# Kernel optimization log

Hardware: AMD Instinct MI355X
Metric: run time of the kernel (lower is better)

## Reference

```python
import jax, jax.numpy as jnp
import numpy as np

B, S, H = 8, 4096, 1024
E, K = 64, 2
CAP_FACTOR = 1.25
TEMP = 1.0
LBW = 0.01


def setup_inputs() -> dict:
    key = jax.random.key(0)
    k1, k2, k3 = jax.random.split(key, 3)
    x = jax.random.normal(k1, (B, S, H), dtype=jnp.float32)
    gate_w = jax.random.normal(k2, (E, H), dtype=jnp.float32) * 0.02
    expert_w = jax.random.normal(k3, (E, H, H), dtype=jnp.float32) * 0.02
    return {"x": x, "gate_w": gate_w, "expert_w": expert_w}


def _moe_forward(x, gate_w, expert_w):
    b, s, h = x.shape
    xf = x.reshape(-1, h)                      # [N, H]
    N = xf.shape[0]
    capacity = int(N * K / E * CAP_FACTOR)

    # --- gating ---
    logits = xf @ gate_w.T                     # [N, E]
    vals, idx = jax.lax.top_k(logits / TEMP, K)  # [N, K]
    probs = jax.nn.softmax(vals, axis=-1)      # [N, K]

    # --- dispatch: first-come-first-served position within each expert ---
    ef = idx.reshape(-1)                       # [N*K], token-major order (matches torch loop)
    onehot = jax.nn.one_hot(ef, E, dtype=jnp.int32)            # [N*K, E]
    pos = jnp.take_along_axis(jnp.cumsum(onehot, axis=0), ef[:, None], axis=1)[:, 0] - 1
    valid = pos < capacity
    slot = jnp.where(valid, ef * capacity + pos, E * capacity)  # out-of-range -> dropped

    # token_map[e, c] = token_idx * K + k  (or -1 if empty)
    token_map = jnp.full((E * capacity,), -1, dtype=jnp.int32)
    token_map = token_map.at[slot].set(jnp.arange(N * K, dtype=jnp.int32), mode="drop")

    tok = jnp.clip(token_map // K, 0, N - 1)
    filled = token_map >= 0
    expert_inputs = jnp.where(filled[:, None], xf[tok], 0.0)    # [E*cap, H]
    expert_inputs = expert_inputs.reshape(E, capacity, h)

    # --- grouped expert GEMM (no bias; zero rows stay zero) ---
    expert_outputs = jnp.einsum("ech,edh->ecd", expert_inputs, expert_w)  # [E, cap, H]

    # --- combine: weighted scatter-add back to tokens ---
    eo_flat = expert_outputs.reshape(E * capacity, h)
    wk = token_map % K
    weight = jnp.where(filled, probs[tok, jnp.clip(wk, 0, K - 1)], 0.0)
    out_idx = jnp.where(filled, tok, N)        # invalid -> dropped
    output = jnp.zeros((N, h), dtype=xf.dtype).at[out_idx].add(
        weight[:, None] * eo_flat, mode="drop")

    # --- aux load-balancing loss ---
    gate_probs = jax.nn.softmax(logits, axis=-1)
    usage = jnp.bincount(ef, length=E).astype(jnp.float32) / (N * K + 1e-9)
    importance = gate_probs.mean(axis=0)
    aux = jnp.sum(usage * importance) * E
    aux = jnp.minimum(aux * LBW, 1.0)

    return output.reshape(b, s, h), aux


def reference(x, gate_w, expert_w):
    return _moe_forward(x, gate_w, expert_w)
```

## Files before the change

### kernel.cpp

```cpp
#include <hip/hip_runtime.h>
#include <hip/hip_bf16.h>

#define NTOK 32768
#define NE 64
#define HD 1024
#define CAP 1280
#define NKF (NTOK*2)
#define NSLOT (NE*CAP)
#define NTILE 128

typedef __attribute__((ext_vector_type(8))) short bf16x8;
typedef __attribute__((ext_vector_type(4))) short bf16x4;
typedef __attribute__((ext_vector_type(4))) float f32x4;
typedef __attribute__((ext_vector_type(4))) unsigned short u16x4;

__device__ __hip_bfloat16 g_zero[1152];

__device__ __forceinline__ short f2bf(float f) {
  union { __hip_bfloat16 b; short s; } u;
  u.b = __float2bfloat16(f);
  return u.s;
}
__device__ __forceinline__ float bf2f(unsigned short h) {
  return __uint_as_float(((unsigned)h) << 16);
}

__global__ __launch_bounds__(256) void gating_kernel(const float* __restrict__ x,
                                                     const float* __restrict__ gw,
                                                     float* __restrict__ logits,
                                                     __hip_bfloat16* __restrict__ xb) {
  __shared__ float Xs[64][132];
  __shared__ float Gs[64][132];
  const int tid = threadIdx.x;
  const int tok0 = blockIdx.x * 64;
  const int th = tid >> 4;
  const int te = tid & 15;
  float acc[4][4];
#pragma unroll
  for (int i = 0; i < 4; ++i)
#pragma unroll
    for (int j = 0; j < 4; ++j) acc[i][j] = 0.f;

  for (int k0 = 0; k0 < HD; k0 += 128) {
#pragma unroll
    for (int r = 0; r < 8; ++r) {
      int idx = r * 256 + tid;
      int row = idx >> 5;
      int c = (idx & 31) * 4;
      float4 xv4 = *(const float4*)&x[(size_t)(tok0 + row) * HD + k0 + c];
      *(float4*)&Xs[row][c] = xv4;
      bf16x4 o;
      o[0] = f2bf(xv4.x); o[1] = f2bf(xv4.y); o[2] = f2bf(xv4.z); o[3] = f2bf(xv4.w);
      *(bf16x4*)&xb[(size_t)(tok0 + row) * HD + k0 + c] = o;
      *(float4*)&Gs[row][c] = *(const float4*)&gw[(size_t)row * HD + k0 + c];
    }
    __syncthreads();
#pragma unroll 4
    for (int kk = 0; kk < 32; ++kk) {
      float4 xv[4], gv[4];
#pragma unroll
      for (int i = 0; i < 4; ++i) xv[i] = *(float4*)&Xs[th + i * 16][kk * 4];
#pragma unroll
      for (int j = 0; j < 4; ++j) gv[j] = *(float4*)&Gs[te + j * 16][kk * 4];
#pragma unroll
      for (int i = 0; i < 4; ++i)
#pragma unroll
        for (int j = 0; j < 4; ++j) {
          acc[i][j] = fmaf(xv[i].x, gv[j].x, acc[i][j]);
          acc[i][j] = fmaf(xv[i].y, gv[j].y, acc[i][j]);
          acc[i][j] = fmaf(xv[i].z, gv[j].z, acc[i][j]);
          acc[i][j] = fmaf(xv[i].w, gv[j].w, acc[i][j]);
        }
    }
    __syncthreads();
  }
#pragma unroll
  for (int i = 0; i < 4; ++i)
#pragma unroll
    for (int j = 0; j < 4; ++j)
      logits[(size_t)(tok0 + th + i * 16) * NE + te + j * 16] = acc[i][j];
}

__global__ __launch_bounds__(256) void topk_hist_kernel(const float* __restrict__ logits,
                                                        int2* __restrict__ e01,
                                                        float2* __restrict__ p01,
                                                        float* __restrict__ imp_part,
                                                        int* __restrict__ rank_buf,
                                                        int* __restrict__ hist) {
  __shared__ int wh[4][64];
  const int tid = threadIdx.x;
  const int w = tid >> 6, lane = tid & 63;
  const int t = blockIdx.x * 256 + tid;
  float l[64];
  const float4* lp = (const float4*)(logits + (size_t)t * NE);
#pragma unroll
  for (int i = 0; i < 16; ++i) {
    float4 v = lp[i];
    l[4 * i] = v.x; l[4 * i + 1] = v.y; l[4 * i + 2] = v.z; l[4 * i + 3] = v.w;
  }
  float v1 = -1e30f; int i1 = 0;
#pragma unroll
  for (int j = 0; j < 64; ++j) if (l[j] > v1) { v1 = l[j]; i1 = j; }
  float v2 = -1e30f; int i2 = 0;
#pragma unroll
  for (int j = 0; j < 64; ++j) if (j != i1 && l[j] > v2) { v2 = l[j]; i2 = j; }
  float ex = __expf(v2 - v1);
  float inv2 = 1.f / (1.f + ex);
  e01[t] = make_int2(i1, i2);
  p01[t] = make_float2(inv2, ex * inv2);

  float s = 0.f;
#pragma unroll
  for (int j = 0; j < 64; ++j) s += __expf(l[j] - v1);
  float invs = 1.f / s;
  const int wid = t >> 6;
#pragma unroll
  for (int e = 0; e < 64; ++e) {
    float p = __expf(l[e] - v1) * invs;
#pragma unroll
    for (int off = 32; off; off >>= 1) p += __shfl_xor(p, off);
    if (lane == 0) imp_part[(size_t)wid * 64 + e] = p;
  }

  int r0 = 0, r1 = 0, cnt = 0;
#pragma unroll
  for (int j = 0; j < 64; ++j) {
    int a = __shfl(i1, j);
    int b = __shfl(i2, j);
    int ja = (j < lane);
    r0 += ja & (a == i1);
    r0 += ja & (b == i1);
    r1 += ja & (a == i2);
    r1 += ja & (b == i2);
    cnt += (a == lane) + (b == lane);
  }
  wh[w][lane] = cnt;
  __syncthreads();
#pragma unroll
  for (int ww = 0; ww < 4; ++ww)
    if (ww < w) { r0 += wh[ww][i1]; r1 += wh[ww][i2]; }
  rank_buf[2 * t] = r0;
  rank_buf[2 * t + 1] = r1;
  if (tid < 64)
    hist[blockIdx.x * 64 + tid] = wh[0][tid] + wh[1][tid] + wh[2][tid] + wh[3][tid];
}

__global__ __launch_bounds__(64) void scan_aux_kernel(const int* __restrict__ hist,
                                                      const float* __restrict__ imp_part,
                                                      int* __restrict__ tile_off,
                                                      int* __restrict__ counts,
                                                      float* __restrict__ out) {
  const int e = threadIdx.x;
  int run = 0;
  for (int t = 0; t < NTILE; ++t) {
    int h = hist[t * 64 + e];
    tile_off[t * 64 + e] = run;
    run += h;
  }
  counts[e] = run;

  float imp = 0.f;
  for (int w = 0; w < 512; ++w) imp += imp_part[(size_t)w * 64 + e];
  imp *= (1.f / (float)NTOK);
  float usage = (float)run / (float)NKF;
  float v = usage * imp;
#pragma unroll
  for (int off = 32; off; off >>= 1) v += __shfl_xor(v, off);
  if (e == 0) out[(size_t)NTOK * HD] = fminf(v * (float)NE * 0.01f, 1.0f);
}

__global__ __launch_bounds__(256) void place_kernel(const int2* __restrict__ e01,
                                                    const int* __restrict__ rank_buf,
                                                    const int* __restrict__ tile_off,
                                                    int* __restrict__ slot_of,
                                                    int* __restrict__ slot_token) {
  const int tid = threadIdx.x;
  const int i = blockIdx.x * 256 + tid;
  int2 ee = e01[i >> 1];
  const int e = (i & 1) ? ee.y : ee.x;
  const int pos = tile_off[(i >> 9) * 64 + e] + rank_buf[i];
  const int slot = (pos < CAP) ? (e * CAP + pos) : -1;
  slot_of[i] = slot;
  if (slot >= 0) slot_token[slot] = i;
}

__global__ __launch_bounds__(256) void convw_kernel(const float* __restrict__ w,
                                                    __hip_bfloat16* __restrict__ wb) {
  size_t i = ((size_t)blockIdx.x * 256 + threadIdx.x) * 8;
  const size_t stride = (size_t)2048 * 256 * 8;
#pragma unroll 2
  for (int it = 0; it < 16; ++it, i += stride) {
    float4 a = *(const float4*)(w + i);
    float4 b = *(const float4*)(w + i + 4);
    bf16x8 o;
    o[0] = f2bf(a.x); o[1] = f2bf(a.y); o[2] = f2bf(a.z); o[3] = f2bf(a.w);
    o[4] = f2bf(b.x); o[5] = f2bf(b.y); o[6] = f2bf(b.z); o[7] = f2bf(b.w);
    *(bf16x8*)(wb + i) = o;
  }
}

#define ASYNC16(g, l) __builtin_amdgcn_global_load_lds( \
    (const __attribute__((address_space(1))) void*)(g), \
    (__attribute__((address_space(3))) void*)(l), 16, 0, 0)

#define STAGE_A(buf, ks, kcol) do {                                             \
    const int _d = ((buf) * 16384 + (ks) * 8192 + wuni) * 2;                    \
    ASYNC16(arow0 + (kcol) + (ks) * 32 + sw8, (char*)lds + _d);                 \
    ASYNC16(arow1 + (kcol) + (ks) * 32 + sw8, (char*)lds + _d + 8192);          \
  } while (0)

#define STAGE_B(buf, ks, kcol) do {                                             \
    const __hip_bfloat16* _g = B + (size_t)srow * HD + (kcol) + (ks) * 32 + sw8; \
    const int _d = (32768 + (buf) * 16384 + (ks) * 8192 + wuni) * 2;            \
    ASYNC16(_g, (char*)lds + _d);                                               \
    ASYNC16(_g + (size_t)128 * HD, (char*)lds + _d + 8192);                     \
  } while (0)

#define LDA(dst, buf, ks, mi) \
  dst = *(const bf16x8*)(lds + (buf) * 16384 + (ks) * 8192 + (wm * 128 + (mi) * 16 + fr) * 32 + rsw)
#define LDB(dst, buf, ks, ni) \
  dst = *(const bf16x8*)(lds + 32768 + (buf) * 16384 + (ks) * 8192 + (wn * 64 + (ni) * 16 + fr) * 32 + rsw)

#define MFMA_HALF(h)                                                            \
  _Pragma("unroll")                                                             \
  for (int mm = 0; mm < 4; ++mm)                                                \
    _Pragma("unroll")                                                           \
    for (int nn = 0; nn < 4; ++nn)                                              \
      acc[(h) * 4 + mm][nn] =                                                   \
          __builtin_amdgcn_mfma_f32_16x16x32_bf16(av[mm], bv[nn], acc[(h) * 4 + mm][nn], 0, 0, 0)

#define BARX() do { asm volatile("" ::: "memory"); __builtin_amdgcn_s_barrier(); asm volatile("" ::: "memory"); } while (0)

__global__ __launch_bounds__(512, 2) void moe_gemm_kernel(const __hip_bfloat16* __restrict__ xb,
                                                          const int* __restrict__ slot_token,
                                                          const __hip_bfloat16* __restrict__ Wb,
                                                          const int* __restrict__ counts,
                                                          __hip_bfloat16* __restrict__ Eo) {
  __shared__ __hip_bfloat16 lds[65536];

  const int bid = blockIdx.x;
  const int swz = (bid & 7) * 160 + (bid >> 3);
  const int e = swz / 20;
  const int t20 = swz - e * 20;
  const int tm = t20 >> 2, tn = t20 & 3;

  const int cnt = counts[e];
  if (tm * 256 >= cnt) return;

  const int tid = threadIdx.x;
  const int lane = tid & 63;
  const int w = tid >> 6;
  const int wm = w >> 2, wn = w & 3;

  const __hip_bfloat16* B = Wb + (size_t)e * HD * HD + (size_t)(tn * 256) * HD;

  const int srow = tid >> 2;
  const int sw8 = ((tid & 3) ^ ((tid >> 3) & 3)) * 8;
  const int wuni = w * 512;

  const int slotbase = e * CAP + tm * 256;
  const int r0row = tm * 256 + srow;
  const int i0 = slot_token[slotbase + srow];
  const int i1 = slot_token[slotbase + 128 + srow];
  const __hip_bfloat16* arow0 = (r0row < cnt) ? xb + (size_t)(i0 >> 1) * HD : g_zero;
  const __hip_bfloat16* arow1 = (r0row + 128 < cnt) ? xb + (size_t)(i1 >> 1) * HD : g_zero;

  const int fr = lane & 15;
  const int fq = lane >> 4;
  const int rsw = (fq ^ ((fr >> 1) & 3)) * 8;

  f32x4 acc[8][4] = {};

  STAGE_A(0, 0, 0);
  STAGE_B(0, 0, 0);
  STAGE_A(0, 1, 0);
  STAGE_B(0, 1, 0);
  asm volatile("s_waitcnt vmcnt(4)" ::: "memory");
  BARX();

#pragma unroll 2
  for (int t = 0; t < 16; ++t) {
    const int cur = t & 1, nxt = cur ^ 1;
    const int kc = (t + 1) * 64;
    const bool hn = (t < 15);
    bf16x8 av[4], bv[4];

    LDB(bv[0], cur, 0, 0); LDB(bv[1], cur, 0, 1); LDB(bv[2], cur, 0, 2); LDB(bv[3], cur, 0, 3);
    LDA(av[0], cur, 0, 0); LDA(av[1], cur, 0, 1); LDA(av[2], cur, 0, 2); LDA(av[3], cur, 0, 3);
    if (hn) STAGE_A(nxt, 0, kc);
    BARX();
    __builtin_amdgcn_s_setprio(1);
    MFMA_HALF(0);
    __builtin_amdgcn_s_setprio(0);
    BARX();

    LDA(av[0], cur, 0, 4); LDA(av[1], cur, 0, 5); LDA(av[2], cur, 0, 6); LDA(av[3], cur, 0, 7);
    if (hn) {
      STAGE_B(nxt, 0, kc);
      asm volatile("s_waitcnt vmcnt(4)" ::: "memory");
    } else {
      asm volatile("s_waitcnt vmcnt(0)" ::: "memory");
    }
    BARX();
    __builtin_amdgcn_s_setprio(1);
    MFMA_HALF(1);
    __builtin_amdgcn_s_setprio(0);
    BARX();

    LDB(bv[0], cur, 1, 0); LDB(bv[1], cur, 1, 1); LDB(bv[2], cur, 1, 2); LDB(bv[3], cur, 1, 3);
    LDA(av[0], cur, 1, 0); LDA(av[1], cur, 1, 1); LDA(av[2], cur, 1, 2); LDA(av[3], cur, 1, 3);
    if (hn) STAGE_A(nxt, 1, kc);
    BARX();
    __builtin_amdgcn_s_setprio(1);
    MFMA_HALF(0);
    __builtin_amdgcn_s_setprio(0);
    BARX();

    LDA(av[0], cur, 1, 4); LDA(av[1], cur, 1, 5); LDA(av[2], cur, 1, 6); LDA(av[3], cur, 1, 7);
    if (hn) {
      STAGE_B(nxt, 1, kc);
      asm volatile("s_waitcnt vmcnt(4)" ::: "memory");
    }
    BARX();
    __builtin_amdgcn_s_setprio(1);
    MFMA_HALF(1);
    __builtin_amdgcn_s_setprio(0);
    BARX();
  }

  __hip_bfloat16* C = Eo + (size_t)e * CAP * HD +
                      (size_t)(tm * 256 + wm * 128) * HD + tn * 256 + wn * 64;
#pragma unroll
  for (int m = 0; m < 8; ++m)
#pragma unroll
    for (int n = 0; n < 4; ++n)
#pragma unroll
      for (int r = 0; r < 4; ++r)
        C[(size_t)(m * 16 + fq * 4 + r) * HD + n * 16 + fr] = __float2bfloat16(acc[m][n][r]);
}

__global__ __launch_bounds__(256) void combine_kernel(const __hip_bfloat16* __restrict__ eo,
                                                      const int* __restrict__ slot_of,
                                                      const float2* __restrict__ p01,
                                                      float* __restrict__ out) {
  const int t = blockIdx.x;
  const int tid = threadIdx.x;
  const float2 p = p01[t];
  const int s0 = slot_of[2 * t], s1 = slot_of[2 * t + 1];
  float a0 = 0.f, a1 = 0.f, a2 = 0.f, a3 = 0.f;
  if (s0 >= 0) {
    u16x4 v = *(const u16x4*)((const unsigned short*)eo + (size_t)s0 * HD + tid * 4);
    a0 += p.x * bf2f(v[0]); a1 += p.x * bf2f(v[1]);
    a2 += p.x * bf2f(v[2]); a3 += p.x * bf2f(v[3]);
  }
  if (s1 >= 0) {
    u16x4 v = *(const u16x4*)((const unsigned short*)eo + (size_t)s1 * HD + tid * 4);
    a0 += p.y * bf2f(v[0]); a1 += p.y * bf2f(v[1]);
    a2 += p.y * bf2f(v[2]); a3 += p.y * bf2f(v[3]);
  }
  float4 res = make_float4(a0, a1, a2, a3);
  *(float4*)(out + (size_t)t * HD + tid * 4) = res;
}

extern "C" void kernel_launch(void* const* d_in, const int* in_sizes, int n_in,
                              void* d_out, int out_size, void* d_ws, size_t ws_size,
                              hipStream_t stream) {
  const float* x = (const float*)d_in[0];
  const float* gw = (const float*)d_in[1];
  const float* ew = (const float*)d_in[2];
  float* out = (float*)d_out;

  char* p = (char*)d_ws;
  float* logits = (float*)p;            p += (size_t)NTOK * NE * 4;
  int2* e01 = (int2*)p;                 p += (size_t)NTOK * 8;
  float2* p01 = (float2*)p;             p += (size_t)NTOK * 8;
  int* slot_of = (int*)p;               p += (size_t)NKF * 4;
  int* slot_token = (int*)p;            p += (size_t)NSLOT * 4;
  int* counts = (int*)p;                p += 256;
  float* imp_part = (float*)p;          p += (size_t)512 * 64 * 4;
  int* rank_buf = (int*)p;              p += (size_t)NKF * 4;
  int* hist = (int*)p;                  p += (size_t)NTILE * 64 * 4;
  int* tile_off = (int*)p;              p += (size_t)NTILE * 64 * 4;
  __hip_bfloat16* xb = (__hip_bfloat16*)p; p += (size_t)NTOK * HD * 2;
  __hip_bfloat16* Wb = (__hip_bfloat16*)p;  p += (size_t)NE * HD * HD * 2;
  __hip_bfloat16* Eo = (__hip_bfloat16*)p;  p += (size_t)NSLOT * HD * 2;

  gating_kernel<<<NTOK / 64, 256, 0, stream>>>(x, gw, logits, xb);
  topk_hist_kernel<<<NTOK / 256, 256, 0, stream>>>(logits, e01, p01, imp_part, rank_buf, hist);
  scan_aux_kernel<<<1, 64, 0, stream>>>(hist, imp_part, tile_off, counts, out);
  place_kernel<<<NKF / 256, 256, 0, stream>>>(e01, rank_buf, tile_off, slot_of, slot_token);
  convw_kernel<<<2048, 256, 0, stream>>>(ew, Wb);
  moe_gemm_kernel<<<dim3(1280), 512, 0, stream>>>(xb, slot_token, Wb, counts, Eo);
  combine_kernel<<<NTOK, 256, 0, stream>>>(Eo, slot_of, p01, out);
}
```

Baseline: 436.7 us.

## Triple-buffer expert weight tiles in LDS to prefetch two K-steps ahead

The B (expert weight) operand in the grouped expert GEMM moves from a double buffer to a three-slot ring in LDS. Weight loads are now issued two K-iterations ahead, while the gathered token rows (A) stay double-buffered one step ahead. The vmcnt wait counts are retuned for the deeper pipeline, including special handling of the last two iterations. This is meant to hide more of the global-load latency for the weights. In exchange, shared memory per block grows from 128 KB to 160 KB, which uses the whole CU's LDS, and the wait accounting becomes more fragile.

```diff
diff --git a/kernel.cpp b/kernel.cpp
--- a/kernel.cpp
+++ b/kernel.cpp
@@ -209,17 +209,17 @@
     ASYNC16(arow1 + (kcol) + (ks) * 32 + sw8, (char*)lds + _d + 8192);          \
   } while (0)
 
-#define STAGE_B(buf, ks, kcol) do {                                             \
+#define STAGE_B3(buf3, ks, kcol) do {                                           \
     const __hip_bfloat16* _g = B + (size_t)srow * HD + (kcol) + (ks) * 32 + sw8; \
-    const int _d = (32768 + (buf) * 16384 + (ks) * 8192 + wuni) * 2;            \
+    const int _d = (32768 + (buf3) * 16384 + (ks) * 8192 + wuni) * 2;           \
     ASYNC16(_g, (char*)lds + _d);                                               \
     ASYNC16(_g + (size_t)128 * HD, (char*)lds + _d + 8192);                     \
   } while (0)
 
 #define LDA(dst, buf, ks, mi) \
   dst = *(const bf16x8*)(lds + (buf) * 16384 + (ks) * 8192 + (wm * 128 + (mi) * 16 + fr) * 32 + rsw)
-#define LDB(dst, buf, ks, ni) \
-  dst = *(const bf16x8*)(lds + 32768 + (buf) * 16384 + (ks) * 8192 + (wn * 64 + (ni) * 16 + fr) * 32 + rsw)
+#define LDB3(dst, buf3, ks, ni) \
+  dst = *(const bf16x8*)(lds + 32768 + (buf3) * 16384 + (ks) * 8192 + (wn * 64 + (ni) * 16 + fr) * 32 + rsw)
 
 #define MFMA_HALF(h)                                                            \
   _Pragma("unroll")                                                             \
@@ -230,13 +230,14 @@
           __builtin_amdgcn_mfma_f32_16x16x32_bf16(av[mm], bv[nn], acc[(h) * 4 + mm][nn], 0, 0, 0)
 
 #define BARX() do { asm volatile("" ::: "memory"); __builtin_amdgcn_s_barrier(); asm volatile("" ::: "memory"); } while (0)
+#define VMC(n) asm volatile("s_waitcnt vmcnt(" #n ")" ::: "memory")
 
 __global__ __launch_bounds__(512, 2) void moe_gemm_kernel(const __hip_bfloat16* __restrict__ xb,
                                                           const int* __restrict__ slot_token,
                                                           const __hip_bfloat16* __restrict__ Wb,
                                                           const int* __restrict__ counts,
                                                           __hip_bfloat16* __restrict__ Eo) {
-  __shared__ __hip_bfloat16 lds[65536];
+  __shared__ __hip_bfloat16 lds[81920];
 
   const int bid = blockIdx.x;
   const int swz = (bid & 7) * 160 + (bid >> 3);
@@ -272,34 +273,42 @@
   f32x4 acc[8][4] = {};
 
   STAGE_A(0, 0, 0);
-  STAGE_B(0, 0, 0);
   STAGE_A(0, 1, 0);
-  STAGE_B(0, 1, 0);
-  asm volatile("s_waitcnt vmcnt(4)" ::: "memory");
+  STAGE_B3(0, 0, 0);
+  STAGE_B3(0, 1, 0);
+  STAGE_B3(1, 0, 64);
+  STAGE_B3(1, 1, 64);
+  VMC(4);
   BARX();
 
 #pragma unroll 2
   for (int t = 0; t < 16; ++t) {
-    const int cur = t & 1, nxt = cur ^ 1;
-    const int kc = (t + 1) * 64;
-    const bool hn = (t < 15);
+    const int ard = t & 1, ast = ard ^ 1;
+    const int b_rd = t % 3;
+    int b_st = b_rd + 2; if (b_st >= 3) b_st -= 3;
+    const int kcA = (t + 1) * 64;
+    const int kcB = (t + 2) * 64;
+    const bool hA = (t < 15);
+    const bool hB = (t < 14);
     bf16x8 av[4], bv[4];
 
-    LDB(bv[0], cur, 0, 0); LDB(bv[1], cur, 0, 1); LDB(bv[2], cur, 0, 2); LDB(bv[3], cur, 0, 3);
-    LDA(av[0], cur, 0, 0); LDA(av[1], cur, 0, 1); LDA(av[2], cur, 0, 2); LDA(av[3], cur, 0, 3);
-    if (hn) STAGE_A(nxt, 0, kc);
+    LDB3(bv[0], b_rd, 0, 0); LDB3(bv[1], b_rd, 0, 1); LDB3(bv[2], b_rd, 0, 2); LDB3(bv[3], b_rd, 0, 3);
+    LDA(av[0], ard, 0, 0); LDA(av[1], ard, 0, 1); LDA(av[2], ard, 0, 2); LDA(av[3], ard, 0, 3);
+    if (hA) STAGE_A(ast, 0, kcA);
     BARX();
     __builtin_amdgcn_s_setprio(1);
     MFMA_HALF(0);
     __builtin_amdgcn_s_setprio(0);
     BARX();
 
-    LDA(av[0], cur, 0, 4); LDA(av[1], cur, 0, 5); LDA(av[2], cur, 0, 6); LDA(av[3], cur, 0, 7);
-    if (hn) {
-      STAGE_B(nxt, 0, kc);
-      asm volatile("s_waitcnt vmcnt(4)" ::: "memory");
+    LDA(av[0], ard, 0, 4); LDA(av[1], ard, 0, 5); LDA(av[2], ard, 0, 6); LDA(av[3], ard, 0, 7);
+    if (hB) {
+      STAGE_B3(b_st, 0, kcB);
+      VMC(6);
+    } else if (t == 14) {
+      VMC(4);
     } else {
-      asm volatile("s_waitcnt vmcnt(0)" ::: "memory");
+      VMC(0);
     }
     BARX();
     __builtin_amdgcn_s_setprio(1);
@@ -307,19 +316,21 @@
     __builtin_amdgcn_s_setprio(0);
     BARX();
 
-    LDB(bv[0], cur, 1, 0); LDB(bv[1], cur, 1, 1); LDB(bv[2], cur, 1, 2); LDB(bv[3], cur, 1, 3);
-    LDA(av[0], cur, 1, 0); LDA(av[1], cur, 1, 1); LDA(av[2], cur, 1, 2); LDA(av[3], cur, 1, 3);
-    if (hn) STAGE_A(nxt, 1, kc);
+    LDB3(bv[0], b_rd, 1, 0); LDB3(bv[1], b_rd, 1, 1); LDB3(bv[2], b_rd, 1, 2); LDB3(bv[3], b_rd, 1, 3);
+    LDA(av[0], ard, 1, 0); LDA(av[1], ard, 1, 1); LDA(av[2], ard, 1, 2); LDA(av[3], ard, 1, 3);
+    if (hA) STAGE_A(ast, 1, kcA);
     BARX();
     __builtin_amdgcn_s_setprio(1);
     MFMA_HALF(0);
     __builtin_amdgcn_s_setprio(0);
     BARX();
 
-    LDA(av[0], cur, 1, 4); LDA(av[1], cur, 1, 5); LDA(av[2], cur, 1, 6); LDA(av[3], cur, 1, 7);
-    if (hn) {
-      STAGE_B(nxt, 1, kc);
-      asm volatile("s_waitcnt vmcnt(4)" ::: "memory");
+    LDA(av[0], ard, 1, 4); LDA(av[1], ard, 1, 5); LDA(av[2], ard, 1, 6); LDA(av[3], ard, 1, 7);
+    if (hB) {
+      STAGE_B3(b_st, 1, kcB);
+      VMC(6);
+    } else if (t == 14) {
+      VMC(2);
     }
     BARX();
     __builtin_amdgcn_s_setprio(1);
```

Measured after the change: 435.6 us. No clear change (-0.3%).
